# Kernel tuning notes

Hardware: AMD Instinct MI355X
Metric: run time of the kernel (lower is better)

The kernel has to match this reference:

```python
import jax, jax.numpy as jnp
import numpy as np
from jax.experimental.ode import odeint

# Physical constants from sfr.__init__
L0 = 0.1      # rest length per segment
D = 0.0075    # tendon offset
DS = 0.005    # arclength step
A_EXT_MAX = 0.04           # max extension used when generating actions
L_MAX = L0 + A_EXT_MAX     # 0.14 -> fixed integration horizon
T = int(round(L_MAX / DS)) + 1  # 29 points: arange(0, L_MAX + DS, DS)
N_SEG = 3
BATCH = 16384


def _ode_fn(y, t):
    # y: [B, 14] = (r:3, R:9 row-major, ux, uy); constant-curvature Cosserat rod
    ux, uy = y[:, 12], y[:, 13]
    R = y[:, 3:12].reshape(-1, 3, 3)
    dr = R[:, :, 2]                      # R @ e3 = third column of R
    z = jnp.zeros_like(ux)
    u_hat = jnp.stack([
        jnp.stack([z, z, uy], axis=-1),
        jnp.stack([z, z, -ux], axis=-1),
        jnp.stack([-uy, ux, z], axis=-1),
    ], axis=-2)                          # [B, 3, 3]
    dR = jnp.einsum('bij,bjk->bik', R, u_hat)
    dz = jnp.zeros((y.shape[0], 2), y.dtype)  # u is constant along s
    return jnp.concatenate([dr, dR.reshape(-1, 9), dz], axis=1)


def setup_inputs() -> dict:
    key = jax.random.key(0)
    k1, k2 = jax.random.split(key)
    ext = jax.random.uniform(k1, (BATCH, N_SEG), dtype=jnp.float32) * A_EXT_MAX
    bend = (jax.random.uniform(k2, (BATCH, N_SEG, 2), dtype=jnp.float32) - 0.5) * 0.02
    actions = jnp.concatenate([ext[:, :, None], bend], axis=-1).reshape(BATCH, 9)
    return {"actions": actions}


def reference(actions):
    B = actions.shape[0]
    t_eval = jnp.arange(T, dtype=jnp.float32) * DS
    # y0 = (r=0, R=I, ux=uy=0)
    y0_base = jnp.concatenate([jnp.zeros(3, jnp.float32),
                               jnp.eye(3, dtype=jnp.float32).reshape(9),
                               jnp.zeros(2, jnp.float32)])
    y0 = jnp.tile(y0_base[None, :], (B, 1))
    row_idx = jnp.arange(T, dtype=jnp.int32)[:, None]  # [T, 1]
    sol_parts = []
    for n in range(N_SEG):
        a = actions[:, 3 * n:3 * n + 3]
        l = L0 + a[:, 0]
        ux = a[:, 2] / (-(l * D))
        uy = a[:, 1] / (l * D)
        y0 = y0.at[:, 12].set(ux).at[:, 13].set(uy)
        sol_b = odeint(_ode_fn, y0, t_eval, rtol=1e-5, atol=1e-7)  # [T, B, 14]
        # hold trajectory constant past each rod's own length (vectorized mask)
        lengths = (l / DS).astype(jnp.int32)                       # [B]
        t_idx = jnp.minimum(row_idx, lengths[None, :])             # [T, B]
        sol_m = jnp.take_along_axis(sol_b, t_idx[:, :, None], axis=0)
        sol_parts.append(sol_m)
        y0 = sol_m[-1]
    return jnp.concatenate(sol_parts, axis=0)  # [3*T, B, 14]
```

## Files before the change

kernel.cpp:

```cpp
#include <hip/hip_runtime.h>


namespace {

constexpr float kL0 = 0.1f;
constexpr float kD  = 0.0075f;
constexpr float kDS = 0.005f;
constexpr int   kT    = 29;
constexpr int   kNSeg = 3;

__device__ __forceinline__ float fast_rcp(float x) {
    return __builtin_amdgcn_rcpf(x);
}

__device__ __forceinline__ void exp_and_p(float ux, float uy, float s,
                                          float E[9], float p[3]) {
    float th2   = ux * ux + uy * uy;
    float theta = sqrtf(th2);
    float A, Bv, c;
    if (theta < 1e-5f) {
        A  = s;
        Bv = 0.5f * s * s;
        c  = 1.0f;
    } else {
        float phi = s * theta;
        float sh, ch;
        __sincosf(0.5f * phi, &sh, &ch);
        float si  = 2.0f * sh * ch;
        float sh2 = 2.0f * sh * sh;
        float rth = fast_rcp(theta);
        A  = si * rth;
        Bv = sh2 * rth * rth;
        c  = 1.0f - sh2;
    }
    float Aux = A * ux, Auy = A * uy;
    E[0] = 1.0f - Bv * uy * uy;
    E[1] = Bv * ux * uy;
    E[2] = Auy;
    E[3] = E[1];
    E[4] = 1.0f - Bv * ux * ux;
    E[5] = -Aux;
    E[6] = -Auy;
    E[7] = Aux;
    E[8] = c;
    p[0] = Bv * uy;
    p[1] = -Bv * ux;
    p[2] = A;
}

__device__ __forceinline__ void seg_state(const float* __restrict__ actions,
                                          int b, int m, int t,
                                          float r[3], float R[9],
                                          float& ux, float& uy) {
    const float a0 = actions[(size_t)b * 9 + 3 * m + 0];
    const float a1 = actions[(size_t)b * 9 + 3 * m + 1];
    const float a2 = actions[(size_t)b * 9 + 3 * m + 2];
    float l  = kL0 + a0;
    float md = l * kD;
    ux = a2 / (-md);
    uy = a1 / md;
    int kmax = (int)(l / kDS);
    int tc = t < kmax ? t : kmax;
    float s = (float)tc * kDS;

    float E[9], p[3];
    exp_and_p(ux, uy, s, E, p);

    float nr[3], NR[9];
#pragma unroll
    for (int i = 0; i < 3; ++i) {
        nr[i] = r[i] + R[3 * i + 0] * p[0] + R[3 * i + 1] * p[1] + R[3 * i + 2] * p[2];
#pragma unroll
        for (int j = 0; j < 3; ++j) {
            NR[3 * i + j] = R[3 * i + 0] * E[j]
                          + R[3 * i + 1] * E[3 + j]
                          + R[3 * i + 2] * E[6 + j];
        }
    }
#pragma unroll
    for (int i = 0; i < 3; ++i) r[i] = nr[i];
#pragma unroll
    for (int i = 0; i < 9; ++i) R[i] = NR[i];
}

__global__ __launch_bounds__(256) void rollout(const float* __restrict__ actions,
                                               float* __restrict__ out, int B) {
    __shared__ float smem[256 * 14];

    int b = blockIdx.x * blockDim.x + threadIdx.x;
    int row = blockIdx.y;
    int n = row / kT;
    int t = row - n * kT;

    float r[3] = {0.f, 0.f, 0.f};
    float R[9] = {1.f, 0.f, 0.f, 0.f, 1.f, 0.f, 0.f, 0.f, 1.f};
    float ux, uy;

    if (n >= 1) seg_state(actions, b, 0, kT, r, R, ux, uy);
    if (n >= 2) seg_state(actions, b, 1, kT, r, R, ux, uy);
    seg_state(actions, b, n, t, r, R, ux, uy);

    float* my = &smem[threadIdx.x * 14];
    my[0] = r[0];  my[1] = r[1];  my[2] = r[2];
#pragma unroll
    for (int i = 0; i < 9; ++i) my[3 + i] = R[i];
    my[12] = ux;
    my[13] = uy;
    __syncthreads();

    size_t blockbase = ((size_t)row * (size_t)B + (size_t)blockIdx.x * 256) * 14;
    float4* o4 = reinterpret_cast<float4*>(out + blockbase);
    const float4* s4 = reinterpret_cast<const float4*>(smem);
#pragma unroll
    for (int k = 0; k < 3; ++k) {
        int q = k * 256 + threadIdx.x;
        o4[q] = s4[q];
    }
    if (threadIdx.x < 128) {
        int q = 768 + threadIdx.x;
        o4[q] = s4[q];
    }
}

}

extern "C" void kernel_launch(void* const* d_in, const int* in_sizes, int n_in,
                              void* d_out, int out_size, void* d_ws, size_t ws_size,
                              hipStream_t stream) {
    const float* actions = (const float*)d_in[0];
    float* out = (float*)d_out;
    int B = in_sizes[0] / 9;
    dim3 block(256);
    dim3 grid((B + 255) / 256, kNSeg * kT);
    rollout<<<grid, block, 0, stream>>>(actions, out, B);
}
```

Baseline: 89.04 us.

## Precompute per-segment base poses in a prep kernel, use nontemporal output stores

Adds a precompute kernel that runs the three segment compositions once per batch element and writes each segment's starting pose, curvatures and clamp index to workspace in SoA layout. The rollout kernel then loads that base state and evaluates only one exponential and composition per output row, instead of recomputing up to three. Output stores become nontemporal. This removes redundant transcendental math and action reads, at the cost of an extra launch and a round trip of about 3 MB through workspace.

```diff
diff --git a/kernel.cpp b/kernel.cpp
--- a/kernel.cpp
+++ b/kernel.cpp
@@ -2,12 +2,15 @@
 
 
 namespace {
+
+typedef float f32x4 __attribute__((ext_vector_type(4)));
 
 constexpr float kL0 = 0.1f;
 constexpr float kD  = 0.0075f;
 constexpr float kDS = 0.005f;
 constexpr int   kT    = 29;
 constexpr int   kNSeg = 3;
+constexpr int   kF    = 16;
 
 __device__ __forceinline__ float fast_rcp(float x) {
     return __builtin_amdgcn_rcpf(x);
@@ -48,57 +51,90 @@
     p[2] = A;
 }
 
-__device__ __forceinline__ void seg_state(const float* __restrict__ actions,
-                                          int b, int m, int t,
-                                          float r[3], float R[9],
-                                          float& ux, float& uy) {
-    const float a0 = actions[(size_t)b * 9 + 3 * m + 0];
-    const float a1 = actions[(size_t)b * 9 + 3 * m + 1];
-    const float a2 = actions[(size_t)b * 9 + 3 * m + 2];
-    float l  = kL0 + a0;
-    float md = l * kD;
-    ux = a2 / (-md);
-    uy = a1 / md;
-    int kmax = (int)(l / kDS);
-    int tc = t < kmax ? t : kmax;
+__device__ __forceinline__ void compose(const float r0[3], const float R0[9],
+                                        const float E[9], const float p[3],
+                                        float r[3], float R[9]) {
+#pragma unroll
+    for (int i = 0; i < 3; ++i) {
+        r[i] = r0[i] + R0[3*i+0] * p[0] + R0[3*i+1] * p[1] + R0[3*i+2] * p[2];
+#pragma unroll
+        for (int j = 0; j < 3; ++j) {
+            R[3*i+j] = R0[3*i+0] * E[j] + R0[3*i+1] * E[3+j] + R0[3*i+2] * E[6+j];
+        }
+    }
+}
+
+__global__ __launch_bounds__(256) void precompute(const float* __restrict__ actions,
+                                                  float* __restrict__ W, int B) {
+    int b = blockIdx.x * 256 + threadIdx.x;
+    if (b >= B) return;
+
+    float r[3] = {0.f, 0.f, 0.f};
+    float R[9] = {1.f, 0.f, 0.f, 0.f, 1.f, 0.f, 0.f, 0.f, 1.f};
+
+#pragma unroll
+    for (int m = 0; m < kNSeg; ++m) {
+        const float a0 = actions[b * 9 + 3 * m + 0];
+        const float a1 = actions[b * 9 + 3 * m + 1];
+        const float a2 = actions[b * 9 + 3 * m + 2];
+        float l   = kL0 + a0;
+        float md  = l * kD;
+        float rmd = fast_rcp(md);
+        float ux  = -a2 * rmd;
+        float uy  = a1 * rmd;
+        int kmax  = (int)(l / kDS);
+
+        size_t base = (size_t)(m * kF) * (size_t)B + (size_t)b;
+        W[base + 0 * (size_t)B] = r[0];
+        W[base + 1 * (size_t)B] = r[1];
+        W[base + 2 * (size_t)B] = r[2];
+#pragma unroll
+        for (int i = 0; i < 9; ++i) W[base + (size_t)(3 + i) * (size_t)B] = R[i];
+        W[base + 12 * (size_t)B] = ux;
+        W[base + 13 * (size_t)B] = uy;
+        W[base + 14 * (size_t)B] = (float)kmax;
+
+        if (m < kNSeg - 1) {
+            float s = (float)kmax * kDS;
+            float E[9], p[3];
+            exp_and_p(ux, uy, s, E, p);
+            float nr[3], NR[9];
+            compose(r, R, E, p, nr, NR);
+#pragma unroll
+            for (int i = 0; i < 3; ++i) r[i] = nr[i];
+#pragma unroll
+            for (int i = 0; i < 9; ++i) R[i] = NR[i];
+        }
+    }
+}
+
+__global__ __launch_bounds__(256) void rollout(const float* __restrict__ W,
+                                               float* __restrict__ out, int B) {
+    __shared__ float smem[256 * 14];
+
+    int b   = blockIdx.x * 256 + threadIdx.x;
+    int row = blockIdx.y;
+    int n   = (row >= 2 * kT) ? 2 : (row >= kT ? 1 : 0);
+    int t   = row - n * kT;
+
+    size_t base = (size_t)(n * kF) * (size_t)B + (size_t)b;
+    float r0[3], R0[9];
+    r0[0] = W[base + 0 * (size_t)B];
+    r0[1] = W[base + 1 * (size_t)B];
+    r0[2] = W[base + 2 * (size_t)B];
+#pragma unroll
+    for (int i = 0; i < 9; ++i) R0[i] = W[base + (size_t)(3 + i) * (size_t)B];
+    float ux = W[base + 12 * (size_t)B];
+    float uy = W[base + 13 * (size_t)B];
+    int kmax = (int)W[base + 14 * (size_t)B];
+
+    int tc  = t < kmax ? t : kmax;
     float s = (float)tc * kDS;
 
     float E[9], p[3];
     exp_and_p(ux, uy, s, E, p);
-
-    float nr[3], NR[9];
-#pragma unroll
-    for (int i = 0; i < 3; ++i) {
-        nr[i] = r[i] + R[3 * i + 0] * p[0] + R[3 * i + 1] * p[1] + R[3 * i + 2] * p[2];
-#pragma unroll
-        for (int j = 0; j < 3; ++j) {
-            NR[3 * i + j] = R[3 * i + 0] * E[j]
-                          + R[3 * i + 1] * E[3 + j]
-                          + R[3 * i + 2] * E[6 + j];
-        }
-    }
-#pragma unroll
-    for (int i = 0; i < 3; ++i) r[i] = nr[i];
-#pragma unroll
-    for (int i = 0; i < 9; ++i) R[i] = NR[i];
-}
-
-__global__ __launch_bounds__(256) void rollout(const float* __restrict__ actions,
-                                               float* __restrict__ out, int B) {
-    __shared__ float smem[256 * 14];
-
-    int b = blockIdx.x * blockDim.x + threadIdx.x;
-    int row = blockIdx.y;
-    int n = row / kT;
-    int t = row - n * kT;
-
-    float r[3] = {0.f, 0.f, 0.f};
-    float R[9] = {1.f, 0.f, 0.f, 0.f, 1.f, 0.f, 0.f, 0.f, 1.f};
-    float ux, uy;
-
-    if (n >= 1) seg_state(actions, b, 0, kT, r, R, ux, uy);
-    if (n >= 2) seg_state(actions, b, 1, kT, r, R, ux, uy);
-    seg_state(actions, b, n, t, r, R, ux, uy);
+    float r[3], R[9];
+    compose(r0, R0, E, p, r, R);
 
     float* my = &smem[threadIdx.x * 14];
     my[0] = r[0];  my[1] = r[1];  my[2] = r[2];
@@ -109,16 +145,16 @@
     __syncthreads();
 
     size_t blockbase = ((size_t)row * (size_t)B + (size_t)blockIdx.x * 256) * 14;
-    float4* o4 = reinterpret_cast<float4*>(out + blockbase);
-    const float4* s4 = reinterpret_cast<const float4*>(smem);
+    f32x4* o4 = reinterpret_cast<f32x4*>(out + blockbase);
+    const f32x4* s4 = reinterpret_cast<const f32x4*>(smem);
 #pragma unroll
     for (int k = 0; k < 3; ++k) {
         int q = k * 256 + threadIdx.x;
-        o4[q] = s4[q];
+        __builtin_nontemporal_store(s4[q], &o4[q]);
     }
     if (threadIdx.x < 128) {
         int q = 768 + threadIdx.x;
-        o4[q] = s4[q];
+        __builtin_nontemporal_store(s4[q], &o4[q]);
     }
 }
 
@@ -129,8 +165,10 @@
                               hipStream_t stream) {
     const float* actions = (const float*)d_in[0];
     float* out = (float*)d_out;
+    float* W   = (float*)d_ws;
     int B = in_sizes[0] / 9;
+
     dim3 block(256);
-    dim3 grid((B + 255) / 256, kNSeg * kT);
-    rollout<<<grid, block, 0, stream>>>(actions, out, B);
+    precompute<<<dim3((B + 255) / 256), block, 0, stream>>>(actions, W, B);
+    rollout<<<dim3((B + 255) / 256, kNSeg * kT), block, 0, stream>>>(W, out, B);
 }
```

Result: slower. 92.73 us (+4.1%).

## Process several time rows per block and stage actions in LDS

Applied to the files above, without the earlier changes.

Each block now covers one segment and a group of about five time rows instead of a single row. The prefix pose from earlier segments is computed once and reused for all of those rows, and the actions chunk is loaded cooperatively into shared memory with vector loads. Output goes out through non-temporal stores. This cuts redundant prefix computation and strided action loads, at the cost of fewer blocks, a serial loop with two barriers per row, and the assumption that B is a multiple of 256.

```diff
diff --git a/kernel.cpp b/kernel.cpp
--- a/kernel.cpp
+++ b/kernel.cpp
@@ -2,12 +2,15 @@
 
 
 namespace {
+
+typedef float f32x4 __attribute__((ext_vector_type(4)));
 
 constexpr float kL0 = 0.1f;
 constexpr float kD  = 0.0075f;
 constexpr float kDS = 0.005f;
 constexpr int   kT    = 29;
 constexpr int   kNSeg = 3;
+constexpr int   kGS   = 6;
 
 __device__ __forceinline__ float fast_rcp(float x) {
     return __builtin_amdgcn_rcpf(x);
@@ -48,77 +51,102 @@
     p[2] = A;
 }
 
-__device__ __forceinline__ void seg_state(const float* __restrict__ actions,
-                                          int b, int m, int t,
-                                          float r[3], float R[9],
-                                          float& ux, float& uy) {
-    const float a0 = actions[(size_t)b * 9 + 3 * m + 0];
-    const float a1 = actions[(size_t)b * 9 + 3 * m + 1];
-    const float a2 = actions[(size_t)b * 9 + 3 * m + 2];
-    float l  = kL0 + a0;
-    float md = l * kD;
-    ux = a2 / (-md);
-    uy = a1 / md;
-    int kmax = (int)(l / kDS);
-    int tc = t < kmax ? t : kmax;
-    float s = (float)tc * kDS;
-
-    float E[9], p[3];
-    exp_and_p(ux, uy, s, E, p);
-
-    float nr[3], NR[9];
+__device__ __forceinline__ void compose(const float r0[3], const float R0[9],
+                                        const float E[9], const float p[3],
+                                        float r[3], float R[9]) {
 #pragma unroll
     for (int i = 0; i < 3; ++i) {
-        nr[i] = r[i] + R[3 * i + 0] * p[0] + R[3 * i + 1] * p[1] + R[3 * i + 2] * p[2];
+        r[i] = r0[i] + R0[3*i+0] * p[0] + R0[3*i+1] * p[1] + R0[3*i+2] * p[2];
 #pragma unroll
         for (int j = 0; j < 3; ++j) {
-            NR[3 * i + j] = R[3 * i + 0] * E[j]
-                          + R[3 * i + 1] * E[3 + j]
-                          + R[3 * i + 2] * E[6 + j];
+            R[3*i+j] = R0[3*i+0] * E[j] + R0[3*i+1] * E[3+j] + R0[3*i+2] * E[6+j];
         }
     }
-#pragma unroll
-    for (int i = 0; i < 3; ++i) r[i] = nr[i];
-#pragma unroll
-    for (int i = 0; i < 9; ++i) R[i] = NR[i];
 }
 
 __global__ __launch_bounds__(256) void rollout(const float* __restrict__ actions,
                                                float* __restrict__ out, int B) {
-    __shared__ float smem[256 * 14];
+    __shared__ float sact[256 * 9];
+    __shared__ float sbuf[256 * 14];
 
-    int b = blockIdx.x * blockDim.x + threadIdx.x;
-    int row = blockIdx.y;
-    int n = row / kT;
-    int t = row - n * kT;
+    const int tid   = threadIdx.x;
+    const int chunk = blockIdx.x;
+    const int n     = blockIdx.y / kGS;
+    const int gs    = blockIdx.y - n * kGS;
+    const int tlo   = (kT * gs) / kGS;
+    const int thi   = (kT * (gs + 1)) / kGS;
 
-    float r[3] = {0.f, 0.f, 0.f};
-    float R[9] = {1.f, 0.f, 0.f, 0.f, 1.f, 0.f, 0.f, 0.f, 1.f};
-    float ux, uy;
-
-    if (n >= 1) seg_state(actions, b, 0, kT, r, R, ux, uy);
-    if (n >= 2) seg_state(actions, b, 1, kT, r, R, ux, uy);
-    seg_state(actions, b, n, t, r, R, ux, uy);
-
-    float* my = &smem[threadIdx.x * 14];
-    my[0] = r[0];  my[1] = r[1];  my[2] = r[2];
-#pragma unroll
-    for (int i = 0; i < 9; ++i) my[3 + i] = R[i];
-    my[12] = ux;
-    my[13] = uy;
+    {
+        const f32x4* a4 = reinterpret_cast<const f32x4*>(
+            actions + (size_t)chunk * 256 * 9);
+        f32x4* s4 = reinterpret_cast<f32x4*>(sact);
+        s4[tid]       = a4[tid];
+        s4[tid + 256] = a4[tid + 256];
+        if (tid < 64) s4[tid + 512] = a4[tid + 512];
+    }
     __syncthreads();
 
-    size_t blockbase = ((size_t)row * (size_t)B + (size_t)blockIdx.x * 256) * 14;
-    float4* o4 = reinterpret_cast<float4*>(out + blockbase);
-    const float4* s4 = reinterpret_cast<const float4*>(smem);
+    float r0[3] = {0.f, 0.f, 0.f};
+    float R0[9] = {1.f, 0.f, 0.f, 0.f, 1.f, 0.f, 0.f, 0.f, 1.f};
+    float sux = 0.f, suy = 0.f;
+    int   skmax = 0;
+
 #pragma unroll
-    for (int k = 0; k < 3; ++k) {
-        int q = k * 256 + threadIdx.x;
-        o4[q] = s4[q];
+    for (int m = 0; m < kNSeg; ++m) {
+        if (m <= n) {
+            const float a0 = sact[tid * 9 + 3 * m + 0];
+            const float a1 = sact[tid * 9 + 3 * m + 1];
+            const float a2 = sact[tid * 9 + 3 * m + 2];
+            float l  = kL0 + a0;
+            float md = l * kD;
+            float ux = a2 / (-md);
+            float uy = a1 / md;
+            int   km = (int)(l / kDS);
+            if (m == n) {
+                sux = ux; suy = uy; skmax = km;
+            } else {
+                float s = (float)km * kDS;
+                float E[9], p[3], nr[3], NR[9];
+                exp_and_p(ux, uy, s, E, p);
+                compose(r0, R0, E, p, nr, NR);
+#pragma unroll
+                for (int i = 0; i < 3; ++i) r0[i] = nr[i];
+#pragma unroll
+                for (int i = 0; i < 9; ++i) R0[i] = NR[i];
+            }
+        }
     }
-    if (threadIdx.x < 128) {
-        int q = 768 + threadIdx.x;
-        o4[q] = s4[q];
+
+    f32x4* sb4 = reinterpret_cast<f32x4*>(sbuf);
+    for (int t = tlo; t < thi; ++t) {
+        int   tc = t < skmax ? t : skmax;
+        float s  = (float)tc * kDS;
+
+        float E[9], p[3], r[3], R[9];
+        exp_and_p(sux, suy, s, E, p);
+        compose(r0, R0, E, p, r, R);
+
+        __syncthreads();
+        float* my = &sbuf[tid * 14];
+        my[0] = r[0];  my[1] = r[1];  my[2] = r[2];
+#pragma unroll
+        for (int i = 0; i < 9; ++i) my[3 + i] = R[i];
+        my[12] = sux;
+        my[13] = suy;
+        __syncthreads();
+
+        size_t base = ((size_t)(n * kT + t) * (size_t)B
+                       + (size_t)chunk * 256) * 14;
+        f32x4* o4 = reinterpret_cast<f32x4*>(out + base);
+#pragma unroll
+        for (int k = 0; k < 3; ++k) {
+            int q = k * 256 + tid;
+            __builtin_nontemporal_store(sb4[q], &o4[q]);
+        }
+        if (tid < 128) {
+            int q = 768 + tid;
+            __builtin_nontemporal_store(sb4[q], &o4[q]);
+        }
     }
 }
 
@@ -131,6 +159,6 @@
     float* out = (float*)d_out;
     int B = in_sizes[0] / 9;
     dim3 block(256);
-    dim3 grid((B + 255) / 256, kNSeg * kT);
+    dim3 grid(B / 256, kNSeg * kGS);
     rollout<<<grid, block, 0, stream>>>(actions, out, B);
 }
```

Result: slower. 91.05 us (+2.3%).
